# Optimization experiments

Measured on AMD Instinct MI355X. Metric: run time of the kernel, lower is better.

Reference implementation:

```python
import jax, jax.numpy as jnp
import numpy as np

B, Z, X = 64, 7, 14
N_T, N_S = Z * Z, X * X
N = N_T + N_S
H, C = 12, 768
HD = C // H
SCALE = HD ** -0.5


def _rpe_index(z, x):
    # concatenated 2D relative positional index for [z,z] template + [x,x] search grids
    zh, zw = np.meshgrid(np.arange(z), np.arange(z), indexing='ij')
    xh, xw = np.meshgrid(np.arange(x), np.arange(x), indexing='ij')
    h = np.concatenate([zh.ravel(), xh.ravel()])
    w = np.concatenate([zw.ravel(), xw.ravel()])
    n = h.shape[0]
    flag = np.zeros(n, dtype=np.int64)
    flag[z * z:] = 1  # 0 = template token, 1 = search token
    key = np.stack([h[:, None] - h[None, :], w[:, None] - w[None, :],
                    np.broadcast_to(flag[None, :], (n, n)),
                    np.broadcast_to(flag[:, None], (n, n))], axis=-1).reshape(-1, 4)
    _, inv = np.unique(key, axis=0, return_inverse=True)
    return inv.reshape(n, n).astype(np.int32)


def setup_inputs() -> dict:
    key = jax.random.key(0)
    ks = jax.random.split(key, 6)
    idx = _rpe_index(Z, X)
    s = 0.02
    return {
        'x': jax.random.normal(ks[0], (B, N, C), jnp.float32),
        'boxmask_vec': jax.random.normal(ks[1], (B, N_T, C), jnp.float32),
        'qkv_w': jax.random.normal(ks[2], (3 * C, C), jnp.float32) * s,
        'qkv_b': jnp.zeros((3 * C,), jnp.float32),
        'proj_w': jax.random.normal(ks[3], (C, C), jnp.float32) * s,
        'proj_b': jnp.zeros((C,), jnp.float32),
        'box_w': jax.random.normal(ks[4], (H, C), jnp.float32) * s,
        'box_b': jnp.zeros((H,), jnp.float32),
        'rpe_table': jax.random.normal(ks[5], (H, int(idx.max()) + 1), jnp.float32) * s,
        'rpe_index': jnp.asarray(idx),
        'lens_t': int(N_T),
    }


def reference(x, boxmask_vec, qkv_w, qkv_b, proj_w, proj_b, box_w, box_b, rpe_table, rpe_index, lens_t):
    Bb, Nn, Cc = x.shape
    qkv = (x @ qkv_w.T + qkv_b).reshape(Bb, Nn, 3, H, HD).transpose(2, 0, 3, 1, 4)
    q, k, v = qkv[0], qkv[1], qkv[2]  # each (B,H,N,hd)
    attn = jnp.einsum('bhid,bhjd->bhij', q, k) * SCALE
    attn = attn + rpe_table[:, rpe_index][None]  # RPE bias gather -> (1,H,N,N)
    lt = lens_t
    rows_t = jnp.arange(Nn)[:, None] < lt
    cols_t = jnp.arange(Nn)[None, :] < lt
    t_mask = (rows_t & cols_t).astype(attn.dtype)  # template-template block
    # Faithful to torch: softmax of (attn * t_mask) over the FULL row; zeros outside the
    # block contribute exp(0)=1 to the denominator. Only template columns matter for the
    # matmul since the expanded boxmask value tensor is zero beyond lens_t rows.
    t_attn = jax.nn.softmax(attn * t_mask, axis=-1)[:, :, :lt, :lt]  # (B,H,lt,lt)
    bm = boxmask_vec.reshape(Bb, lt, H, HD).transpose(0, 2, 1, 3)    # (B,H,lt,hd)
    out_t = jnp.einsum('bhij,bhjd->bhid', t_attn, bm)                # (B,H,lt,hd)
    t_vec = out_t.transpose(0, 2, 1, 3).reshape(Bb, lt, Cc)
    factor = (t_vec @ box_w.T + box_b).transpose(0, 2, 1)            # (B,H,lt)
    fac_rows = jnp.pad(factor, ((0, 0), (0, 0), (0, Nn - lt)))       # (B,H,N)
    ts_mask = rows_t & (~cols_t)  # template-rows -> search-cols block
    attn = jnp.where(ts_mask[None, None], attn * fac_rows[..., None], attn)
    attn = jax.nn.softmax(attn, axis=-1)
    out = jnp.einsum('bhij,bhjd->bhid', attn, v).transpose(0, 2, 1, 3).reshape(Bb, Nn, Cc)
    return out @ proj_w.T + proj_b
```

## Files before the change

kernel.cpp:

```cpp
#include <hip/hip_runtime.h>
#include <hip/hip_bf16.h>

#define B_ 64
#define N_ 245
#define NT_ 49
#define H_ 12
#define HD_ 64
#define C_ 768
#define C3_ 2304
#define M_ (B_*N_)
#define MP_ 15744
#define MB_ 123
#define KB_ 24
#define SCALE_ 0.125f
#define RPE_MAX_ 1792
#define NPAD_ 256

typedef short short8 __attribute__((ext_vector_type(8)));
typedef float f32x4 __attribute__((ext_vector_type(4)));
typedef ushort us8 __attribute__((ext_vector_type(8)));
typedef ushort us4 __attribute__((ext_vector_type(4)));

__device__ __forceinline__ ushort f2bf(float f) {
  unsigned u = __builtin_bit_cast(unsigned, f);
  u += 0x7fffu + ((u >> 16) & 1u);
  return (ushort)(u >> 16);
}
__device__ __forceinline__ float bf2f(ushort u) {
  return __builtin_bit_cast(float, ((unsigned)u) << 16);
}
__device__ __forceinline__ void split2(float a, ushort& hi, ushort& lo) {
  unsigned u = __builtin_bit_cast(unsigned, a);
  hi = (ushort)(u >> 16);
  float hf = __builtin_bit_cast(float, u & 0xffff0000u);
  lo = (ushort)(__builtin_bit_cast(unsigned, a - hf) >> 16);
}

__global__ __launch_bounds__(256) void split_img_kernel(
    const float* __restrict__ A, ushort* __restrict__ img, int rows, int K, int total)
{
  int idx = blockIdx.x*256 + threadIdx.x;
  if (idx >= total) return;
  const int ch = idx & 3;
  const int r  = (idx >> 2) & 127;
  const int t  = idx >> 9;
  const int KBl = K >> 5;
  const int kb = t % KBl, mb = t / KBl;
  const int m = mb*128 + r;
  float4 v0 = make_float4(0,0,0,0), v1 = make_float4(0,0,0,0);
  if (m < rows) {
    const float* p = A + (size_t)m*K + kb*32 + ch*8;
    v0 = *(const float4*)p; v1 = *(const float4*)(p+4);
  }
  float vals[8] = {v0.x,v0.y,v0.z,v0.w,v1.x,v1.y,v1.z,v1.w};
  us8 hv, lv;
  #pragma unroll
  for (int e = 0; e < 8; ++e) { ushort hh, ll; split2(vals[e], hh, ll); hv[e]=hh; lv[e]=ll; }
  ushort* base = img + ((size_t)t*128 + r)*64;
  const int sw = (ch ^ (r&7))*8;
  *(us8*)(base + sw)        = hv;
  *(us8*)(base + (sw ^ 32)) = lv;
}

__device__ __forceinline__ void stage_tile(const ushort* __restrict__ src, ushort* dst,
                                           int wid, int lane) {
  #pragma unroll
  for (int t = 0; t < 4; ++t) {
    const int o = (wid*4 + t) * 512;
    __builtin_amdgcn_global_load_lds(
      (const __attribute__((address_space(1))) unsigned int*)(src + o + lane*8),
      (__attribute__((address_space(3))) unsigned int*)(dst + o),
      16, 0, 0);
  }
}

__global__ __launch_bounds__(256) void gemm3_kernel(
    const ushort* __restrict__ Aimg, const ushort* __restrict__ Bimg,
    const float* __restrict__ bias, float* __restrict__ Co,
    int KB, int Nn, int M)
{
  __shared__ __align__(16) ushort lds[2][16384];
  const int tid = threadIdx.x, lane = tid & 63, wid = tid >> 6;
  const int g = lane >> 4, li = lane & 15;
  const int nb = blockIdx.x, mb = blockIdx.y;
  const int wr = (wid >> 1) * 64, wc = (wid & 1) * 64;

  const ushort* Abase = Aimg + (size_t)mb * KB * 8192;
  const ushort* Bbase = Bimg + (size_t)nb * KB * 8192;

  f32x4 acc[4][4];
  #pragma unroll
  for (int i = 0; i < 4; ++i)
    #pragma unroll
    for (int j = 0; j < 4; ++j) acc[i][j] = (f32x4){0.f,0.f,0.f,0.f};

  stage_tile(Abase, &lds[0][0],    wid, lane);
  stage_tile(Bbase, &lds[0][8192], wid, lane);
  __syncthreads();

  for (int kb = 0; kb < KB; ++kb) {
    const int cur = kb & 1;
    if (kb + 1 < KB) {
      stage_tile(Abase + (size_t)(kb+1)*8192, &lds[cur^1][0],    wid, lane);
      stage_tile(Bbase + (size_t)(kb+1)*8192, &lds[cur^1][8192], wid, lane);
    }
    short8 ah[4], al[4], bh[4], bl[4];
    #pragma unroll
    for (int t = 0; t < 4; ++t) {
      const int ra = wr + t*16 + li;
      const ushort* Ar = &lds[cur][ra*64];
      const int ca = (g ^ (ra & 7)) * 8;
      ah[t] = *(const short8*)(Ar + ca);
      al[t] = *(const short8*)(Ar + (ca ^ 32));
      const int rb = wc + t*16 + li;
      const ushort* Br = &lds[cur][8192 + rb*64];
      const int cb = (g ^ (rb & 7)) * 8;
      bh[t] = *(const short8*)(Br + cb);
      bl[t] = *(const short8*)(Br + (cb ^ 32));
    }
    #pragma unroll
    for (int i = 0; i < 4; ++i)
      #pragma unroll
      for (int j = 0; j < 4; ++j) {
        acc[i][j] = __builtin_amdgcn_mfma_f32_16x16x32_bf16(ah[i], bh[j], acc[i][j], 0,0,0);
        acc[i][j] = __builtin_amdgcn_mfma_f32_16x16x32_bf16(al[i], bh[j], acc[i][j], 0,0,0);
        acc[i][j] = __builtin_amdgcn_mfma_f32_16x16x32_bf16(ah[i], bl[j], acc[i][j], 0,0,0);
      }
    __syncthreads();
  }

  #pragma unroll
  for (int i = 0; i < 4; ++i) {
    const int m0 = mb*128 + wr + i*16 + g*4;
    #pragma unroll
    for (int j = 0; j < 4; ++j) {
      const int n = nb*128 + wc + j*16 + li;
      const float bv = bias[n];
      #pragma unroll
      for (int rr = 0; rr < 4; ++rr) {
        const int m = m0 + rr;
        if (m < M) Co[(size_t)m * Nn + n] = acc[i][j][rr] + bv;
      }
    }
  }
}

__global__ __launch_bounds__(256) void gemm3_qkv_kernel(
    const ushort* __restrict__ Aimg, const ushort* __restrict__ Bimg,
    const float* __restrict__ bias,
    ushort* __restrict__ Qimg, ushort* __restrict__ Kimg, ushort* __restrict__ VTimg,
    int KB)
{
  __shared__ __align__(16) ushort lds[2][16384];
  const int tid = threadIdx.x, lane = tid & 63, wid = tid >> 6;
  const int g = lane >> 4, li = lane & 15;
  const int mb = blockIdx.x, nb = blockIdx.y;
  const int wr = (wid >> 1) * 64, wc = (wid & 1) * 64;

  const ushort* Abase = Aimg + (size_t)mb * KB * 8192;
  const ushort* Bbase = Bimg + (size_t)nb * KB * 8192;

  f32x4 acc[4][4];
  #pragma unroll
  for (int i = 0; i < 4; ++i)
    #pragma unroll
    for (int j = 0; j < 4; ++j) acc[i][j] = (f32x4){0.f,0.f,0.f,0.f};

  stage_tile(Abase, &lds[0][0],    wid, lane);
  stage_tile(Bbase, &lds[0][8192], wid, lane);
  __syncthreads();

  for (int kb = 0; kb < KB; ++kb) {
    const int cur = kb & 1;
    if (kb + 1 < KB) {
      stage_tile(Abase + (size_t)(kb+1)*8192, &lds[cur^1][0],    wid, lane);
      stage_tile(Bbase + (size_t)(kb+1)*8192, &lds[cur^1][8192], wid, lane);
    }
    short8 ah[4], al[4], bh[4], bl[4];
    #pragma unroll
    for (int t = 0; t < 4; ++t) {
      const int ra = wr + t*16 + li;
      const ushort* Ar = &lds[cur][ra*64];
      const int ca = (g ^ (ra & 7)) * 8;
      ah[t] = *(const short8*)(Ar + ca);
      al[t] = *(const short8*)(Ar + (ca ^ 32));
      const int rb = wc + t*16 + li;
      const ushort* Br = &lds[cur][8192 + rb*64];
      const int cb = (g ^ (rb & 7)) * 8;
      bh[t] = *(const short8*)(Br + cb);
      bl[t] = *(const short8*)(Br + (cb ^ 32));
    }
    #pragma unroll
    for (int i = 0; i < 4; ++i)
      #pragma unroll
      for (int j = 0; j < 4; ++j) {
        acc[i][j] = __builtin_amdgcn_mfma_f32_16x16x32_bf16(ah[i], bh[j], acc[i][j], 0,0,0);
        acc[i][j] = __builtin_amdgcn_mfma_f32_16x16x32_bf16(al[i], bh[j], acc[i][j], 0,0,0);
        acc[i][j] = __builtin_amdgcn_mfma_f32_16x16x32_bf16(ah[i], bl[j], acc[i][j], 0,0,0);
      }
    __syncthreads();
  }

  #pragma unroll
  for (int i = 0; i < 4; ++i) {
    const int ch0 = mb*128 + wr + i*16 + g*4;
    const int part = ch0 / 768;
    const int rem  = ch0 - part*768;
    const int h = rem >> 6, d0 = rem & 63;
    const float b0 = bias[ch0+0], b1 = bias[ch0+1], b2 = bias[ch0+2], b3 = bias[ch0+3];
    #pragma unroll
    for (int j = 0; j < 4; ++j) {
      const int tok = nb*128 + wc + j*16 + li;
      if (tok < M_) {
        const int b = tok / 245;
        const int jl = tok - b*245;
        const int bh = b*H_ + h;
        if (part == 0) {
          us4 q4 = { f2bf((acc[i][j][0] + b0)*SCALE_), f2bf((acc[i][j][1] + b1)*SCALE_),
                     f2bf((acc[i][j][2] + b2)*SCALE_), f2bf((acc[i][j][3] + b3)*SCALE_) };
          *(us4*)(Qimg + ((size_t)bh*NPAD_ + jl)*64 + d0) = q4;
        } else if (part == 1) {
          us4 k4 = { f2bf(acc[i][j][0] + b0), f2bf(acc[i][j][1] + b1),
                     f2bf(acc[i][j][2] + b2), f2bf(acc[i][j][3] + b3) };
          *(us4*)(Kimg + ((size_t)bh*NPAD_ + jl)*64 + (d0 ^ ((jl&7)<<3))) = k4;
        } else {
          VTimg[((size_t)bh*64 + d0+0)*NPAD_ + (jl ^ (((d0+0)&7)<<3))] = f2bf(acc[i][j][0] + b0);
          VTimg[((size_t)bh*64 + d0+1)*NPAD_ + (jl ^ (((d0+1)&7)<<3))] = f2bf(acc[i][j][1] + b1);
          VTimg[((size_t)bh*64 + d0+2)*NPAD_ + (jl ^ (((d0+2)&7)<<3))] = f2bf(acc[i][j][2] + b2);
          VTimg[((size_t)bh*64 + d0+3)*NPAD_ + (jl ^ (((d0+3)&7)<<3))] = f2bf(acc[i][j][3] + b3);
        }
      }
    }
  }
}

__global__ __launch_bounds__(256) void g_kernel(
    const float* __restrict__ boxmask, const float* __restrict__ box_w,
    float* __restrict__ G)
{
  __shared__ float bms[NT_][65];
  __shared__ float bws[H_][65];
  const int bx = blockIdx.x;
  const int b = bx / H_, ht = bx % H_;
  const int tid = threadIdx.x;
  for (int idx = tid; idx < NT_*64; idx += 256) {
    int j = idx >> 6, d = idx & 63;
    bms[j][d] = boxmask[((size_t)(b*NT_ + j))*C_ + ht*64 + d];
  }
  for (int idx = tid; idx < H_*64; idx += 256) {
    int h = idx >> 6, d = idx & 63;
    bws[h][d] = box_w[(size_t)h*C_ + ht*64 + d];
  }
  __syncthreads();
  for (int o = tid; o < H_*64; o += 256) {
    int h = o >> 6, j = o & 63;
    float s = 0.f;
    if (j < NT_) {
      #pragma unroll
      for (int d = 0; d < 64; ++d) s = fmaf(bws[h][d], bms[j][d], s);
    }
    G[(size_t)bx*H_*64 + o] = s;
  }
}

__global__ __launch_bounds__(256) void tmpl_kernel(
    const ushort* __restrict__ Qimg, const ushort* __restrict__ Kimg,
    const float* __restrict__ G, const float* __restrict__ biasT,
    float* __restrict__ F_part)
{
  __shared__ __align__(16) ushort kt_lds[64*64];
  __shared__ __align__(16) float Gs[H_*64];
  const int bx = blockIdx.x;
  const int b = bx / H_, ht = bx % H_;
  const int tid = threadIdx.x, lane = tid & 63, wid = tid >> 6;
  const int g = lane >> 4, li = lane & 15;

  const ushort* Kb = Kimg + (size_t)bx*NPAD_*64;
  #pragma unroll
  for (int t = 0; t < 2; ++t) {
    const int o = (t*4 + wid) * 512;
    __builtin_amdgcn_global_load_lds(
      (const __attribute__((address_space(1))) unsigned int*)(Kb + o + lane*8),
      (__attribute__((address_space(3))) unsigned int*)(kt_lds + o), 16, 0, 0);
  }
  for (int idx = tid; idx < H_*64; idx += 256) Gs[idx] = G[(size_t)bx*H_*64 + idx];

  const int i = wid*16 + li;
  short8 bq[2];
  {
    const ushort* qp = Qimg + ((size_t)bx*NPAD_ + i)*64;
    bq[0] = *(const short8*)(qp + g*8);
    bq[1] = *(const short8*)(qp + 32 + g*8);
  }
  __syncthreads();

  f32x4 sacc[4];
  #pragma unroll
  for (int jt = 0; jt < 4; ++jt) sacc[jt] = (f32x4){0.f,0.f,0.f,0.f};
  #pragma unroll
  for (int jt = 0; jt < 4; ++jt) {
    int jr = jt*16 + li;
    #pragma unroll
    for (int kc = 0; kc < 2; ++kc) {
      short8 af = *(const short8*)(kt_lds + jr*64 + ((kc*32 + g*8) ^ ((jr&7)<<3)));
      sacc[jt] = __builtin_amdgcn_mfma_f32_16x16x32_bf16(af, bq[kc], sacc[jt], 0, 0, 0);
    }
  }

  const float* bT = biasT + (size_t)ht*NPAD_*NPAD_;
  float mloc = 0.f;
  #pragma unroll
  for (int jt = 0; jt < 4; ++jt)
    #pragma unroll
    for (int r = 0; r < 4; ++r) {
      int j = jt*16 + g*4 + r;
      float sv = (j < NT_) ? (sacc[jt][r] + bT[(size_t)j*NPAD_ + i]) : -1e30f;
      sacc[jt][r] = sv;
      mloc = fmaxf(mloc, sv);
    }
  mloc = fmaxf(mloc, __shfl_xor(mloc, 16));
  mloc = fmaxf(mloc, __shfl_xor(mloc, 32));
  float ssum = 0.f;
  #pragma unroll
  for (int jt = 0; jt < 4; ++jt)
    #pragma unroll
    for (int r = 0; r < 4; ++r) {
      int j = jt*16 + g*4 + r;
      float e = (j < NT_) ? __expf(sacc[jt][r] - mloc) : 0.f;
      sacc[jt][r] = e;
      ssum += e;
    }
  ssum += __shfl_xor(ssum, 16);
  ssum += __shfl_xor(ssum, 32);
  const float inv = 1.f / (ssum + 196.f * __expf(-mloc));

  float F[12];
  #pragma unroll
  for (int h = 0; h < 12; ++h) F[h] = 0.f;
  #pragma unroll
  for (int jt = 0; jt < 4; ++jt) {
    f32x4 p = sacc[jt] * inv;
    #pragma unroll
    for (int h = 0; h < 12; ++h) {
      const float4 g4 = *(const float4*)(&Gs[h*64 + jt*16 + g*4]);
      F[h] = fmaf(p[0], g4.x, fmaf(p[1], g4.y, fmaf(p[2], g4.z, fmaf(p[3], g4.w, F[h]))));
    }
  }
  #pragma unroll
  for (int h = 0; h < 12; ++h) {
    F[h] += __shfl_xor(F[h], 16);
    F[h] += __shfl_xor(F[h], 32);
  }
  if (lane < 16 && i < NT_) {
    #pragma unroll
    for (int h = 0; h < 12; ++h)
      F_part[((size_t)(b*H_ + h)*NT_ + i)*12 + ht] = F[h];
  }
}

__global__ __launch_bounds__(256) void bias_kernel(
    const float* __restrict__ rpe_table, const int* __restrict__ rpe_index,
    float* __restrict__ biasT, int rpe_m)
{
  int idx = blockIdx.x * 256 + threadIdx.x;
  if (idx >= H_*N_*N_) return;
  int h = idx / (N_*N_);
  int rem = idx % (N_*N_);
  int j = rem / N_;
  int i = rem % N_;
  biasT[((size_t)h*NPAD_ + j)*NPAD_ + i] = rpe_table[h*rpe_m + rpe_index[i*N_ + j]];
}

__global__ __launch_bounds__(256) void attn_mfma_kernel(
    const ushort* __restrict__ Qimg, const ushort* __restrict__ Kimg,
    const ushort* __restrict__ VTimg, const float* __restrict__ biasT,
    const float* __restrict__ F_part, const float* __restrict__ box_b,
    ushort* __restrict__ attnimg)
{
  __shared__ __align__(16) ushort kp_lds[NPAD_*64];
  __shared__ __align__(16) ushort vt_lds[64*NPAD_];
  const int bx = blockIdx.x;
  const int bh = bx >> 2, rb = bx & 3;
  const int b = bh / H_, h = bh % H_;
  const int tid = threadIdx.x, lane = tid & 63, wid = tid >> 6;
  const int g = lane >> 4, li = lane & 15;

  const ushort* Kb = Kimg  + (size_t)bh*16384;
  const ushort* Vb = VTimg + (size_t)bh*16384;
  #pragma unroll
  for (int t = 0; t < 8; ++t) {
    const int o = (t*4 + wid) * 512;
    __builtin_amdgcn_global_load_lds(
      (const __attribute__((address_space(1))) unsigned int*)(Kb + o + lane*8),
      (__attribute__((address_space(3))) unsigned int*)(kp_lds + o), 16, 0, 0);
    __builtin_amdgcn_global_load_lds(
      (const __attribute__((address_space(1))) unsigned int*)(Vb + o + lane*8),
      (__attribute__((address_space(3))) unsigned int*)(vt_lds + o), 16, 0, 0);
  }

  const int i0 = rb*64 + wid*16;
  const int ig = i0 + li;
  const int iq = (ig < N_) ? ig : (N_-1);
  short8 bq[2];
  {
    const ushort* qp = Qimg + ((size_t)bh*NPAD_ + iq)*64;
    bq[0] = *(const short8*)(qp + g*8);
    bq[1] = *(const short8*)(qp + 32 + g*8);
  }
  __syncthreads();

  f32x4 sacc[16];
  #pragma unroll
  for (int jt = 0; jt < 16; ++jt) sacc[jt] = (f32x4){0.f,0.f,0.f,0.f};
  #pragma unroll
  for (int jt = 0; jt < 16; ++jt) {
    int jr = jt*16 + li;
    #pragma unroll
    for (int kc = 0; kc < 2; ++kc) {
      short8 af = *(const short8*)(kp_lds + jr*64 + ((kc*32 + g*8) ^ ((jr&7)<<3)));
      sacc[jt] = __builtin_amdgcn_mfma_f32_16x16x32_bf16(af, bq[kc], sacc[jt], 0, 0, 0);
    }
  }
  __syncthreads();

  float fac = 1.0f;
  if (ig < NT_) {
    const float* fp = F_part + ((size_t)bh*NT_ + ig)*12;
    float4 f0 = *(const float4*)fp;
    float4 f1 = *(const float4*)(fp+4);
    float4 f2 = *(const float4*)(fp+8);
    fac = box_b[h] + f0.x+f0.y+f0.z+f0.w + f1.x+f1.y+f1.z+f1.w + f2.x+f2.y+f2.z+f2.w;
  }
  const float* bT = biasT + (size_t)h*NPAD_*NPAD_;
  float mloc = -1e30f;
  #pragma unroll
  for (int jt = 0; jt < 16; ++jt) {
    #pragma unroll
    for (int r = 0; r < 4; ++r) {
      int j = jt*16 + g*4 + r;
      float sv = sacc[jt][r] + bT[(size_t)j*NPAD_ + i0 + li];
      if (ig < NT_ && j >= NT_) sv *= fac;
      if (j >= N_) sv = -1e30f;
      sacc[jt][r] = sv;
      mloc = fmaxf(mloc, sv);
    }
  }
  mloc = fmaxf(mloc, __shfl_xor(mloc, 16));
  mloc = fmaxf(mloc, __shfl_xor(mloc, 32));
  float ssum = 0.f;
  #pragma unroll
  for (int jt = 0; jt < 16; ++jt) {
    #pragma unroll
    for (int r = 0; r < 4; ++r) {
      float e = __expf(sacc[jt][r] - mloc);
      sacc[jt][r] = e;
      ssum += e;
    }
  }
  ssum += __shfl_xor(ssum, 16);
  ssum += __shfl_xor(ssum, 32);
  const float inv = 1.0f / ssum;

  ushort* pbase = kp_lds + wid*4096 + li*256;
  const int swz = (li & 7) << 3;
  #pragma unroll
  for (int jt = 0; jt < 16; ++jt) {
    unsigned w0 = (unsigned)f2bf(sacc[jt][0]*inv) | ((unsigned)f2bf(sacc[jt][1]*inv) << 16);
    unsigned w1 = (unsigned)f2bf(sacc[jt][2]*inv) | ((unsigned)f2bf(sacc[jt][3]*inv) << 16);
    *(uint2*)(pbase + ((jt*16 + g*4) ^ swz)) = make_uint2(w0, w1);
  }

  f32x4 oacc[4];
  #pragma unroll
  for (int dt = 0; dt < 4; ++dt) oacc[dt] = (f32x4){0.f,0.f,0.f,0.f};
  #pragma unroll
  for (int jc = 0; jc < 8; ++jc) {
    short8 pf = *(const short8*)(pbase + ((jc*32 + g*8) ^ swz));
    #pragma unroll
    for (int dt = 0; dt < 4; ++dt) {
      int row = dt*16 + li;
      short8 vf = *(const short8*)(vt_lds + row*NPAD_ + ((jc*32 + g*8) ^ ((row&7)<<3)));
      oacc[dt] = __builtin_amdgcn_mfma_f32_16x16x32_bf16(vf, pf, oacc[dt], 0, 0, 0);
    }
  }
  __syncthreads();

  float* tb = (float*)(kp_lds + wid*4096);
  #pragma unroll
  for (int dt = 0; dt < 4; ++dt)
    #pragma unroll
    for (int rr = 0; rr < 4; ++rr)
      tb[(dt*16 + g*4 + rr)*19 + li] = oacc[dt][rr];

  const int rtok = lane >> 2, cg = lane & 3;
  const int tokl = i0 + rtok;
  if (tokl < N_) {
    const int m = b*N_ + tokl;
    const int mbm = m >> 7, rr_ = m & 127, rx = rr_ & 7;
    const int kbb = h*2 + (cg >> 1);
    ushort* baseimg = attnimg + (((size_t)(mbm*KB_ + kbb))*128 + rr_)*64;
    #pragma unroll
    for (int half = 0; half < 2; ++half) {
      us8 hv, lv;
      #pragma unroll
      for (int e = 0; e < 8; ++e) {
        float v = tb[(cg*16 + half*8 + e)*19 + rtok];
        ushort hh, ll; split2(v, hh, ll);
        hv[e] = hh; lv[e] = ll;
      }
      const int c0 = (cg & 1)*2 + half;
      *(us8*)(baseimg + ((c0 ^ rx) * 8))        = hv;
      *(us8*)(baseimg + (((c0 ^ 4) ^ rx) * 8))  = lv;
    }
  }
}

extern "C" void kernel_launch(void* const* d_in, const int* in_sizes, int n_in,
                              void* d_out, int out_size, void* d_ws, size_t ws_size,
                              hipStream_t stream)
{
  const float* x         = (const float*)d_in[0];
  const float* boxmask   = (const float*)d_in[1];
  const float* qkv_w     = (const float*)d_in[2];
  const float* qkv_b     = (const float*)d_in[3];
  const float* proj_w    = (const float*)d_in[4];
  const float* proj_b    = (const float*)d_in[5];
  const float* box_w     = (const float*)d_in[6];
  const float* box_b     = (const float*)d_in[7];
  const float* rpe_table = (const float*)d_in[8];
  const int*   rpe_index = (const int*)d_in[9];
  const int rpe_m = in_sizes[8] / H_;

  float* ws      = (float*)d_ws;
  float* G       = ws;
  float* F_part  = G + (size_t)B_*H_*H_*64;
  float* biasT   = F_part + (size_t)B_*H_*NT_*12;
  ushort* ximg    = (ushort*)(biasT + (size_t)H_*NPAD_*NPAD_);
  ushort* wqkvimg  = ximg     + (size_t)MP_*C_*2;
  ushort* wprojimg = wqkvimg  + (size_t)C3_*C_*2;
  ushort* Qimg     = wprojimg + (size_t)C_*C_*2;
  ushort* Kimg     = Qimg     + (size_t)B_*H_*NPAD_*64;
  ushort* VTimg    = Kimg     + (size_t)B_*H_*NPAD_*64;
  ushort* attnimg  = ximg;
  float* out     = (float*)d_out;

  bias_kernel<<<(H_*N_*N_ + 255)/256, 256, 0, stream>>>(rpe_table, rpe_index, biasT, rpe_m);
  g_kernel<<<B_*H_, 256, 0, stream>>>(boxmask, box_w, G);
  split_img_kernel<<<(MB_*KB_*512 + 255)/256, 256, 0, stream>>>(x, ximg, M_, C_, MB_*KB_*512);
  split_img_kernel<<<(18*KB_*512 + 255)/256, 256, 0, stream>>>(qkv_w, wqkvimg, C3_, C_, 18*KB_*512);
  split_img_kernel<<<(6*KB_*512 + 255)/256, 256, 0, stream>>>(proj_w, wprojimg, C_, C_, 6*KB_*512);
  gemm3_qkv_kernel<<<dim3(C3_/128, MB_), 256, 0, stream>>>(wqkvimg, ximg, qkv_b, Qimg, Kimg, VTimg, KB_);
  tmpl_kernel<<<B_*H_, 256, 0, stream>>>(Qimg, Kimg, G, biasT, F_part);
  attn_mfma_kernel<<<B_*H_*4, 256, 0, stream>>>(Qimg, Kimg, VTimg, biasT, F_part, box_b, attnimg);
  gemm3_kernel<<<dim3(C_/128, MB_), 256, 0, stream>>>(attnimg, wprojimg, proj_b, out, KB_, C_, M_);
}
```

Baseline: 440.3 us.

## Fuse prep kernels, swizzle GEMM blocks across XCDs, store RPE bias as bf16

Merges the bias gather, G computation and three split-image launches into one prep kernel, which removes several launches. Both GEMMs now take a 1D grid remapped with an XCD-aware swizzle so neighbouring tiles share an L2. The RPE bias table is stored in bf16 to halve its footprint. The attention kernel now reads V fragments straight from global memory instead of staging them in LDS, which lowers LDS use and may raise occupancy but puts the V reads on the global path and rounds the bias.

```diff
diff --git a/kernel.cpp b/kernel.cpp
--- a/kernel.cpp
+++ b/kernel.cpp
@@ -13,8 +13,9 @@
 #define MB_ 123
 #define KB_ 24
 #define SCALE_ 0.125f
-#define RPE_MAX_ 1792
 #define NPAD_ 256
+#define NWG_QKV_ (18*123)
+#define NWG_PROJ_ (6*123)
 
 typedef short short8 __attribute__((ext_vector_type(8)));
 typedef float f32x4 __attribute__((ext_vector_type(4)));
@@ -35,12 +36,15 @@
   float hf = __builtin_bit_cast(float, u & 0xffff0000u);
   lo = (ushort)(__builtin_bit_cast(unsigned, a - hf) >> 16);
 }
-
-__global__ __launch_bounds__(256) void split_img_kernel(
-    const float* __restrict__ A, ushort* __restrict__ img, int rows, int K, int total)
-{
-  int idx = blockIdx.x*256 + threadIdx.x;
-  if (idx >= total) return;
+__device__ __forceinline__ int xcd_swz(int orig, int nwg) {
+  const int q = nwg >> 3, r = nwg & 7;
+  const int xcd = orig & 7, off = orig >> 3;
+  return (xcd < r ? xcd*(q+1) : r*(q+1) + (xcd-r)*q) + off;
+}
+
+__device__ __forceinline__ void split_dev(
+    const float* __restrict__ A, ushort* __restrict__ img, int rows, int K, int idx)
+{
   const int ch = idx & 3;
   const int r  = (idx >> 2) & 127;
   const int t  = idx >> 9;
@@ -62,6 +66,63 @@
   *(us8*)(base + (sw ^ 32)) = lv;
 }
 
+#define PREP_X_   5904
+#define PREP_WQ_  864
+#define PREP_WP_  288
+#define PREP_BT_  2814
+#define PREP_G_   768
+__global__ __launch_bounds__(256) void prep_kernel(
+    const float* __restrict__ x, const float* __restrict__ qkv_w,
+    const float* __restrict__ proj_w, const float* __restrict__ rpe_table,
+    const int* __restrict__ rpe_index, const float* __restrict__ boxmask,
+    const float* __restrict__ box_w,
+    ushort* __restrict__ ximg, ushort* __restrict__ wqkvimg, ushort* __restrict__ wprojimg,
+    ushort* __restrict__ biasTb, float* __restrict__ G, int rpe_m)
+{
+  __shared__ float bms[NT_][65];
+  __shared__ float bws[H_][65];
+  int id = blockIdx.x;
+  const int tid = threadIdx.x;
+  if (id < PREP_X_)  { split_dev(x,      ximg,     M_,  C_, id*256 + tid); return; }
+  id -= PREP_X_;
+  if (id < PREP_WQ_) { split_dev(qkv_w,  wqkvimg,  C3_, C_, id*256 + tid); return; }
+  id -= PREP_WQ_;
+  if (id < PREP_WP_) { split_dev(proj_w, wprojimg, C_,  C_, id*256 + tid); return; }
+  id -= PREP_WP_;
+  if (id < PREP_BT_) {
+    int idx = id*256 + tid;
+    if (idx < H_*N_*N_) {
+      int h = idx / (N_*N_);
+      int rem = idx % (N_*N_);
+      int j = rem / N_, i = rem % N_;
+      biasTb[((size_t)h*NPAD_ + j)*NPAD_ + i] = f2bf(rpe_table[h*rpe_m + rpe_index[i*N_ + j]]);
+    }
+    return;
+  }
+  id -= PREP_BT_;
+  {
+    const int b = id / H_, ht = id % H_;
+    for (int idx = tid; idx < NT_*64; idx += 256) {
+      int j = idx >> 6, d = idx & 63;
+      bms[j][d] = boxmask[((size_t)(b*NT_ + j))*C_ + ht*64 + d];
+    }
+    for (int idx = tid; idx < H_*64; idx += 256) {
+      int h = idx >> 6, d = idx & 63;
+      bws[h][d] = box_w[(size_t)h*C_ + ht*64 + d];
+    }
+    __syncthreads();
+    for (int o = tid; o < H_*64; o += 256) {
+      int h = o >> 6, j = o & 63;
+      float s = 0.f;
+      if (j < NT_) {
+        #pragma unroll
+        for (int d = 0; d < 64; ++d) s = fmaf(bws[h][d], bms[j][d], s);
+      }
+      G[(size_t)id*H_*64 + o] = s;
+    }
+  }
+}
+
 __device__ __forceinline__ void stage_tile(const ushort* __restrict__ src, ushort* dst,
                                            int wid, int lane) {
   #pragma unroll
@@ -82,7 +143,8 @@
   __shared__ __align__(16) ushort lds[2][16384];
   const int tid = threadIdx.x, lane = tid & 63, wid = tid >> 6;
   const int g = lane >> 4, li = lane & 15;
-  const int nb = blockIdx.x, mb = blockIdx.y;
+  const int sid = xcd_swz(blockIdx.x, NWG_PROJ_);
+  const int nb = sid % 6, mb = sid / 6;
   const int wr = (wid >> 1) * 64, wc = (wid & 1) * 64;
 
   const ushort* Abase = Aimg + (size_t)mb * KB * 8192;
@@ -154,7 +216,8 @@
   __shared__ __align__(16) ushort lds[2][16384];
   const int tid = threadIdx.x, lane = tid & 63, wid = tid >> 6;
   const int g = lane >> 4, li = lane & 15;
-  const int mb = blockIdx.x, nb = blockIdx.y;
+  const int sid = xcd_swz(blockIdx.x, NWG_QKV_);
+  const int mb = sid % 18, nb = sid / 18;
   const int wr = (wid >> 1) * 64, wc = (wid & 1) * 64;
 
   const ushort* Abase = Aimg + (size_t)mb * KB * 8192;
@@ -234,38 +297,9 @@
   }
 }
 
-__global__ __launch_bounds__(256) void g_kernel(
-    const float* __restrict__ boxmask, const float* __restrict__ box_w,
-    float* __restrict__ G)
-{
-  __shared__ float bms[NT_][65];
-  __shared__ float bws[H_][65];
-  const int bx = blockIdx.x;
-  const int b = bx / H_, ht = bx % H_;
-  const int tid = threadIdx.x;
-  for (int idx = tid; idx < NT_*64; idx += 256) {
-    int j = idx >> 6, d = idx & 63;
-    bms[j][d] = boxmask[((size_t)(b*NT_ + j))*C_ + ht*64 + d];
-  }
-  for (int idx = tid; idx < H_*64; idx += 256) {
-    int h = idx >> 6, d = idx & 63;
-    bws[h][d] = box_w[(size_t)h*C_ + ht*64 + d];
-  }
-  __syncthreads();
-  for (int o = tid; o < H_*64; o += 256) {
-    int h = o >> 6, j = o & 63;
-    float s = 0.f;
-    if (j < NT_) {
-      #pragma unroll
-      for (int d = 0; d < 64; ++d) s = fmaf(bws[h][d], bms[j][d], s);
-    }
-    G[(size_t)bx*H_*64 + o] = s;
-  }
-}
-
 __global__ __launch_bounds__(256) void tmpl_kernel(
     const ushort* __restrict__ Qimg, const ushort* __restrict__ Kimg,
-    const float* __restrict__ G, const float* __restrict__ biasT,
+    const float* __restrict__ G, const ushort* __restrict__ biasTb,
     float* __restrict__ F_part)
 {
   __shared__ __align__(16) ushort kt_lds[64*64];
@@ -307,14 +341,14 @@
     }
   }
 
-  const float* bT = biasT + (size_t)ht*NPAD_*NPAD_;
+  const ushort* bT = biasTb + (size_t)ht*NPAD_*NPAD_;
   float mloc = 0.f;
   #pragma unroll
   for (int jt = 0; jt < 4; ++jt)
     #pragma unroll
     for (int r = 0; r < 4; ++r) {
       int j = jt*16 + g*4 + r;
-      float sv = (j < NT_) ? (sacc[jt][r] + bT[(size_t)j*NPAD_ + i]) : -1e30f;
+      float sv = (j < NT_) ? (sacc[jt][r] + bf2f(bT[(size_t)j*NPAD_ + i])) : -1e30f;
       sacc[jt][r] = sv;
       mloc = fmaxf(mloc, sv);
     }
@@ -358,27 +392,13 @@
   }
 }
 
-__global__ __launch_bounds__(256) void bias_kernel(
-    const float* __restrict__ rpe_table, const int* __restrict__ rpe_index,
-    float* __restrict__ biasT, int rpe_m)
-{
-  int idx = blockIdx.x * 256 + threadIdx.x;
-  if (idx >= H_*N_*N_) return;
-  int h = idx / (N_*N_);
-  int rem = idx % (N_*N_);
-  int j = rem / N_;
-  int i = rem % N_;
-  biasT[((size_t)h*NPAD_ + j)*NPAD_ + i] = rpe_table[h*rpe_m + rpe_index[i*N_ + j]];
-}
-
 __global__ __launch_bounds__(256) void attn_mfma_kernel(
     const ushort* __restrict__ Qimg, const ushort* __restrict__ Kimg,
-    const ushort* __restrict__ VTimg, const float* __restrict__ biasT,
+    const ushort* __restrict__ VTimg, const ushort* __restrict__ biasTb,
     const float* __restrict__ F_part, const float* __restrict__ box_b,
     ushort* __restrict__ attnimg)
 {
   __shared__ __align__(16) ushort kp_lds[NPAD_*64];
-  __shared__ __align__(16) ushort vt_lds[64*NPAD_];
   const int bx = blockIdx.x;
   const int bh = bx >> 2, rb = bx & 3;
   const int b = bh / H_, h = bh % H_;
@@ -393,9 +413,6 @@
     __builtin_amdgcn_global_load_lds(
       (const __attribute__((address_space(1))) unsigned int*)(Kb + o + lane*8),
       (__attribute__((address_space(3))) unsigned int*)(kp_lds + o), 16, 0, 0);
-    __builtin_amdgcn_global_load_lds(
-      (const __attribute__((address_space(1))) unsigned int*)(Vb + o + lane*8),
-      (__attribute__((address_space(3))) unsigned int*)(vt_lds + o), 16, 0, 0);
   }
 
   const int i0 = rb*64 + wid*16;
@@ -431,14 +448,14 @@
     float4 f2 = *(const float4*)(fp+8);
     fac = box_b[h] + f0.x+f0.y+f0.z+f0.w + f1.x+f1.y+f1.z+f1.w + f2.x+f2.y+f2.z+f2.w;
   }
-  const float* bT = biasT + (size_t)h*NPAD_*NPAD_;
+  const ushort* bT = biasTb + (size_t)h*NPAD_*NPAD_;
   float mloc = -1e30f;
   #pragma unroll
   for (int jt = 0; jt < 16; ++jt) {
     #pragma unroll
     for (int r = 0; r < 4; ++r) {
       int j = jt*16 + g*4 + r;
-      float sv = sacc[jt][r] + bT[(size_t)j*NPAD_ + i0 + li];
+      float sv = sacc[jt][r] + bf2f(bT[(size_t)j*NPAD_ + i0 + li]);
       if (ig < NT_ && j >= NT_) sv *= fac;
       if (j >= N_) sv = -1e30f;
       sacc[jt][r] = sv;
@@ -479,11 +496,10 @@
     #pragma unroll
     for (int dt = 0; dt < 4; ++dt) {
       int row = dt*16 + li;
-      short8 vf = *(const short8*)(vt_lds + row*NPAD_ + ((jc*32 + g*8) ^ ((row&7)<<3)));
+      short8 vf = *(const short8*)(Vb + row*NPAD_ + ((jc*32 + g*8) ^ ((row&7)<<3)));
       oacc[dt] = __builtin_amdgcn_mfma_f32_16x16x32_bf16(vf, pf, oacc[dt], 0, 0, 0);
     }
   }
-  __syncthreads();
 
   float* tb = (float*)(kp_lds + wid*4096);
   #pragma unroll
@@ -534,8 +550,8 @@
   float* ws      = (float*)d_ws;
   float* G       = ws;
   float* F_part  = G + (size_t)B_*H_*H_*64;
-  float* biasT   = F_part + (size_t)B_*H_*NT_*12;
-  ushort* ximg    = (ushort*)(biasT + (size_t)H_*NPAD_*NPAD_);
+  ushort* biasTb = (ushort*)(F_part + (size_t)B_*H_*NT_*12);
+  ushort* ximg    = biasTb   + (size_t)H_*NPAD_*NPAD_;
   ushort* wqkvimg  = ximg     + (size_t)MP_*C_*2;
   ushort* wprojimg = wqkvimg  + (size_t)C3_*C_*2;
   ushort* Qimg     = wprojimg + (size_t)C_*C_*2;
@@ -544,13 +560,11 @@
   ushort* attnimg  = ximg;
   float* out     = (float*)d_out;
 
-  bias_kernel<<<(H_*N_*N_ + 255)/256, 256, 0, stream>>>(rpe_table, rpe_index, biasT, rpe_m);
-  g_kernel<<<B_*H_, 256, 0, stream>>>(boxmask, box_w, G);
-  split_img_kernel<<<(MB_*KB_*512 + 255)/256, 256, 0, stream>>>(x, ximg, M_, C_, MB_*KB_*512);
-  split_img_kernel<<<(18*KB_*512 + 255)/256, 256, 0, stream>>>(qkv_w, wqkvimg, C3_, C_, 18*KB_*512);
-  split_img_kernel<<<(6*KB_*512 + 255)/256, 256, 0, stream>>>(proj_w, wprojimg, C_, C_, 6*KB_*512);
-  gemm3_qkv_kernel<<<dim3(C3_/128, MB_), 256, 0, stream>>>(wqkvimg, ximg, qkv_b, Qimg, Kimg, VTimg, KB_);
-  tmpl_kernel<<<B_*H_, 256, 0, stream>>>(Qimg, Kimg, G, biasT, F_part);
-  attn_mfma_kernel<<<B_*H_*4, 256, 0, stream>>>(Qimg, Kimg, VTimg, biasT, F_part, box_b, attnimg);
-  gemm3_kernel<<<dim3(C_/128, MB_), 256, 0, stream>>>(attnimg, wprojimg, proj_b, out, KB_, C_, M_);
-}
+  prep_kernel<<<PREP_X_+PREP_WQ_+PREP_WP_+PREP_BT_+PREP_G_, 256, 0, stream>>>(
+      x, qkv_w, proj_w, rpe_table, rpe_index, boxmask, box_w,
+      ximg, wqkvimg, wprojimg, biasTb, G, rpe_m);
+  gemm3_qkv_kernel<<<NWG_QKV_, 256, 0, stream>>>(wqkvimg, ximg, qkv_b, Qimg, Kimg, VTimg, KB_);
+  tmpl_kernel<<<B_*H_, 256, 0, stream>>>(Qimg, Kimg, G, biasTb, F_part);
+  attn_mfma_kernel<<<B_*H_*4, 256, 0, stream>>>(Qimg, Kimg, VTimg, biasTb, F_part, box_b, attnimg);
+  gemm3_kernel<<<NWG_PROJ_, 256, 0, stream>>>(attnimg, wprojimg, proj_b, out, KB_, C_, M_);
+}
```

Measured after the change: 418.8 us. 4.9% less time.
